# Kernel tuning notes

Hardware: AMD Instinct MI355X
Metric: run time of the kernel (lower is better)

## Reference

```python
import jax, jax.numpy as jnp
import numpy as np

EPS = 1e-7  # K.epsilon()
ROUTINGS = 3


def squash(v, axis=-1):
    s2 = jnp.sum(jnp.square(v), axis=axis, keepdims=True)
    scale = s2 / (1.0 + s2) / jnp.sqrt(s2 + EPS)
    return scale * v


def setup_inputs() -> dict:
    key = jax.random.key(0)
    k1, k2 = jax.random.split(key)
    B, Ni, Di, No, Do = 64, 2048, 16, 32, 16
    inputs = jax.random.normal(k1, (B, Ni, Di), dtype=jnp.float32)
    # glorot-uniform-ish scale for W
    limit = np.sqrt(6.0 / (Di + Do)).astype(np.float32)
    W = jax.random.uniform(k2, (1, Ni, No, Do, Di), dtype=jnp.float32,
                           minval=-limit, maxval=limit)
    return {"inputs": inputs, "W": W}


def reference(inputs, W):
    # inputs: [B, Ni, Di]; W: [1, Ni, No, Do, Di]
    # inputs_hat[b,n,o,d] = sum_i W[n,o,d,i] * inputs[b,n,i]  -> [B, Ni, No, Do]
    inputs_hat = jnp.einsum('bni,nodi->bnod', inputs, W[0])
    B, Ni, No, _ = inputs_hat.shape
    b = jnp.zeros((B, Ni, No), dtype=inputs_hat.dtype)
    outputs = None
    for i in range(ROUTINGS):
        c = jax.nn.softmax(b, axis=2)              # [B, Ni, No]
        s = jnp.einsum('bnod,bno->bod', inputs_hat, c)  # weighted sum over Ni
        outputs = squash(s)                        # [B, No, Do]
        if i < ROUTINGS - 1:
            # NOTE: faithful to source — update uses sum over Do of c-weighted
            # inputs_hat (does NOT use `outputs`).
            b = b + jnp.sum(inputs_hat * c[..., None], axis=-1)
    return outputs
```

## Files before the change

kernel.cpp:

```cpp
#include <hip/hip_runtime.h>
#include <cmath>


#define NI 2048
#define NGROUPS 256
#define NPER 8

typedef short bf16x8 __attribute__((ext_vector_type(8)));
typedef float f32x4 __attribute__((ext_vector_type(4)));

static __device__ __forceinline__ unsigned cvt_pk_bf16(float a, float b) {
  unsigned r;
  asm("v_cvt_pk_bf16_f32 %0, %1, %2" : "=v"(r) : "v"(a), "v"(b));
  return r;
}
static __device__ __forceinline__ void split4_pk(float4 v, uint2& hi, uint2& lo) {
  hi.x = cvt_pk_bf16(v.x, v.y);
  hi.y = cvt_pk_bf16(v.z, v.w);
  float r0 = v.x - __uint_as_float(hi.x << 16);
  float r1 = v.y - __uint_as_float(hi.x & 0xFFFF0000u);
  float r2 = v.z - __uint_as_float(hi.y << 16);
  float r3 = v.w - __uint_as_float(hi.y & 0xFFFF0000u);
  lo.x = cvt_pk_bf16(r0, r1);
  lo.y = cvt_pk_bf16(r2, r3);
}
static __device__ __forceinline__ int swz8(int r, int u) {
  return r * 8 + ((u ^ ((r >> 2) & 1)) << 2);
}

#define WAOFF 0
#define XBOFF 8192
#define HOFF  8704
#define C2OFF 9760
#define LDSZ  10816
__global__ __launch_bounds__(512, 4) void caps_fused_kernel(
    const float* __restrict__ x, const float* __restrict__ W,
    float* __restrict__ partial)
{
  const int bx = blockIdx.x;
  const int xcd = bx & 7, slot = bx >> 3;
  const int ng = xcd * 32 + (slot >> 1);
  const int bh = slot & 1;
  const int t = threadIdx.x;
  const int wv = t >> 6, l = t & 63;
  const int q = l >> 4, dq = l & 15, qh = q & 1, s_a = q >> 1;
  const int bt = wv & 1, oq = wv >> 1;

  __shared__ __align__(16) float lds[LDSZ];
  float* WA  = lds + WAOFF;
  float* XB  = lds + XBOFF;
  float* hS  = lds + HOFF;
  float* c2S = lds + C2OFF;

  float sacc[8][4];
  #pragma unroll
  for (int oo = 0; oo < 8; ++oo)
    { sacc[oo][0] = 0.f; sacc[oo][1] = 0.f; sacc[oo][2] = 0.f; sacc[oo][3] = 0.f; }

  const int n0 = ng * NPER;
  const int wd = (t >> 2) & 15, wi4 = t & 3;
  const int wu = wi4 >> 1, wsub = (wi4 & 1) * 2;
  const int xb = t >> 2, xi4 = t & 3;
  const int xu = xi4 >> 1, xsub = (xi4 & 1) * 2;

  float4 wreg[4];
  float4 xreg = make_float4(0.f, 0.f, 0.f, 0.f);
  #pragma unroll
  for (int c = 0; c < 4; ++c)
    wreg[c] = *(const float4*)(W + (size_t)n0 * 8192 + c * 2048 + 4 * t);
  if (t < 128)
    xreg = *(const float4*)(x + (size_t)(bh * 32 + xb) * (NI * 16) + n0 * 16 + xi4 * 4);

  #pragma unroll
  for (int c = 0; c < 4; ++c) {
    uint2 hi, lo;
    split4_pk(wreg[c], hi, lo);
    const int rh = (c * 8 + wv) * 32 + wd;
    *(uint2*)&WA[swz8(rh, wu) + wsub] = hi;
    *(uint2*)&WA[swz8(rh + 16, wu) + wsub] = lo;
  }
  if (t < 128) {
    uint2 hi, lo;
    split4_pk(xreg, hi, lo);
    *(uint2*)&XB[swz8(xb, xu) + xsub] = hi;
    *(uint2*)&XB[swz8(32 + xb, xu) + xsub] = lo;
  }
  __syncthreads();

  {
    const size_t nb = (size_t)(n0 + 1);
    #pragma unroll
    for (int c = 0; c < 4; ++c)
      wreg[c] = *(const float4*)(W + nb * 8192 + c * 2048 + 4 * t);
    if (t < 128)
      xreg = *(const float4*)(x + (size_t)(bh * 32 + xb) * (NI * 16) + nb * 16 + xi4 * 4);
  }

  #pragma unroll 1
  for (int nn = 0; nn < NPER; ++nn) {
    f32x4 Dv[8];
    {
      bf16x8 B0 = *(const bf16x8*)&XB[swz8(bt * 16 + dq, qh)];
      bf16x8 B1 = *(const bf16x8*)&XB[swz8(32 + bt * 16 + dq, qh)];
      #pragma unroll
      for (int oo = 0; oo < 8; ++oo) {
        const int o = oq * 8 + oo;
        bf16x8 A = *(const bf16x8*)&WA[swz8(o * 32 + s_a * 16 + dq, qh)];
        f32x4 D = {0.f, 0.f, 0.f, 0.f};
        D = __builtin_amdgcn_mfma_f32_16x16x32_bf16(A, B0, D, 0, 0, 0);
        D = __builtin_amdgcn_mfma_f32_16x16x32_bf16(A, B1, D, 0, 0, 0);
        Dv[oo] = D;
        float hs = D[0] + D[1] + D[2] + D[3];
        hs += __shfl_xor(hs, 16);
        hs += __shfl_xor(hs, 32);
        if (q == 0) hS[(bt * 16 + dq) * 33 + o] = hs;
      }
    }
    __syncthreads();

    if (nn < NPER - 1) {
      #pragma unroll
      for (int c = 0; c < 4; ++c) {
        uint2 hi, lo;
        split4_pk(wreg[c], hi, lo);
        const int rh = (c * 8 + wv) * 32 + wd;
        *(uint2*)&WA[swz8(rh, wu) + wsub] = hi;
        *(uint2*)&WA[swz8(rh + 16, wu) + wsub] = lo;
      }
      if (t < 128) {
        uint2 hi, lo;
        split4_pk(xreg, hi, lo);
        *(uint2*)&XB[swz8(xb, xu) + xsub] = hi;
        *(uint2*)&XB[swz8(32 + xb, xu) + xsub] = lo;
      }
    }

    {
      const int bl = t >> 4, op = t & 15;
      const float h0 = hS[bl * 33 + op];
      const float h1 = hS[bl * 33 + op + 16];
      const float b10 = h0 * 0.03125f, b11 = h1 * 0.03125f;
      float mx = fmaxf(b10, b11);
      mx = fmaxf(mx, __shfl_xor(mx, 1)); mx = fmaxf(mx, __shfl_xor(mx, 2));
      mx = fmaxf(mx, __shfl_xor(mx, 4)); mx = fmaxf(mx, __shfl_xor(mx, 8));
      const float e0 = __expf(b10 - mx), e1 = __expf(b11 - mx);
      float S = e0 + e1;
      S += __shfl_xor(S, 1); S += __shfl_xor(S, 2);
      S += __shfl_xor(S, 4); S += __shfl_xor(S, 8);
      const float inv = 1.0f / S;
      const float b20 = b10 + e0 * inv * h0, b21 = b11 + e1 * inv * h1;
      float mx2 = fmaxf(b20, b21);
      mx2 = fmaxf(mx2, __shfl_xor(mx2, 1)); mx2 = fmaxf(mx2, __shfl_xor(mx2, 2));
      mx2 = fmaxf(mx2, __shfl_xor(mx2, 4)); mx2 = fmaxf(mx2, __shfl_xor(mx2, 8));
      const float e20 = __expf(b20 - mx2), e21 = __expf(b21 - mx2);
      float S2 = e20 + e21;
      S2 += __shfl_xor(S2, 1); S2 += __shfl_xor(S2, 2);
      S2 += __shfl_xor(S2, 4); S2 += __shfl_xor(S2, 8);
      const float inv2 = 1.0f / S2;
      c2S[op * 33 + bl] = e20 * inv2;
      c2S[(op + 16) * 33 + bl] = e21 * inv2;
    }

    if (nn < NPER - 2) {
      const size_t nb = (size_t)(n0 + nn + 2);
      #pragma unroll
      for (int c = 0; c < 4; ++c)
        wreg[c] = *(const float4*)(W + nb * 8192 + c * 2048 + 4 * t);
      if (t < 128)
        xreg = *(const float4*)(x + (size_t)(bh * 32 + xb) * (NI * 16) + nb * 16 + xi4 * 4);
    }
    __syncthreads();

    #pragma unroll
    for (int oo = 0; oo < 8; ++oo) {
      const int o = oq * 8 + oo;
      const float c = c2S[o * 33 + bt * 16 + dq];
      sacc[oo][0] += c * Dv[oo][0]; sacc[oo][1] += c * Dv[oo][1];
      sacc[oo][2] += c * Dv[oo][2]; sacc[oo][3] += c * Dv[oo][3];
    }
  }

  float* pb = partial + (size_t)ng * 32768
            + (size_t)(bh * 32 + bt * 16 + dq) * 512 + q * 4;
  #pragma unroll
  for (int oo = 0; oo < 8; ++oo) {
    const int o = oq * 8 + oo;
    *(float4*)(pb + o * 16)
        = make_float4(sacc[oo][0], sacc[oo][1], sacc[oo][2], sacc[oo][3]);
  }
}

__global__ __launch_bounds__(256) void caps_reduce_kernel(
    const float* __restrict__ partial, float* __restrict__ out)
{
  const int t = threadIdx.x;
  const int w4 = t >> 6, ln = t & 63;
  const int pair = blockIdx.x * 4 + w4;
  const int b = pair >> 5, o = pair & 31;
  const int d = ln & 15, cg = ln >> 4;
  const float* p = partial + (size_t)b * 512 + o * 16 + d;
  float s = 0.f;
  #pragma unroll 8
  for (int gg = cg; gg < NGROUPS; gg += 4) s += p[(size_t)gg * 32768];
  s += __shfl_xor(s, 16); s += __shfl_xor(s, 32);
  float s2 = s * s;
  s2 += __shfl_xor(s2, 1); s2 += __shfl_xor(s2, 2);
  s2 += __shfl_xor(s2, 4); s2 += __shfl_xor(s2, 8);
  float scale = s2 / (1.0f + s2) / sqrtf(s2 + 1e-7f);
  if (ln < 16) out[(size_t)b * 512 + o * 16 + d] = scale * s;
}

extern "C" void kernel_launch(void* const* d_in, const int* in_sizes, int n_in,
                              void* d_out, int out_size, void* d_ws, size_t ws_size,
                              hipStream_t stream) {
  const float* x = (const float*)d_in[0];
  const float* W = (const float*)d_in[1];
  if (in_sizes[0] != 64 * 2048 * 16) { const float* tmp = x; x = W; W = tmp; }
  float* out = (float*)d_out;

  float* partial = (float*)d_ws;

  caps_fused_kernel<<<512, 512, 0, stream>>>(x, W, partial);
  caps_reduce_kernel<<<512, 256, 0, stream>>>(partial, out);
}
```

Baseline: 125.0 us.

## Preload all x slices into LDS upfront, raise MFMA priority, widen reduce kernel

The fused kernel now loads and bf16-splits the x tiles for all eight capsules of a group into LDS once at the start, instead of streaming one per iteration through registers with only 128 threads. The MFMA section is wrapped in s_setprio to favour matrix issue. The reduce kernel gives each (b,o) pair its own 256-thread block and sums through an LDS tree, so it issues more parallel loads across a 4x larger grid. The larger LDS footprint may lower occupancy, and the startup load adds latency before the first compute.

```diff
diff --git a/kernel.cpp b/kernel.cpp
--- a/kernel.cpp
+++ b/kernel.cpp
@@ -29,10 +29,10 @@
 }
 
 #define WAOFF 0
-#define XBOFF 8192
-#define HOFF  8704
-#define C2OFF 9760
-#define LDSZ  10816
+#define XLOFF 8192
+#define HOFF  12288
+#define C2OFF 13344
+#define LDSZ  14400
 __global__ __launch_bounds__(512, 4) void caps_fused_kernel(
     const float* __restrict__ x, const float* __restrict__ W,
     float* __restrict__ partial)
@@ -48,7 +48,7 @@
 
   __shared__ __align__(16) float lds[LDSZ];
   float* WA  = lds + WAOFF;
-  float* XB  = lds + XBOFF;
+  float* XL  = lds + XLOFF;
   float* hS  = lds + HOFF;
   float* c2S = lds + C2OFF;
 
@@ -60,16 +60,25 @@
   const int n0 = ng * NPER;
   const int wd = (t >> 2) & 15, wi4 = t & 3;
   const int wu = wi4 >> 1, wsub = (wi4 & 1) * 2;
-  const int xb = t >> 2, xi4 = t & 3;
-  const int xu = xi4 >> 1, xsub = (xi4 & 1) * 2;
 
   float4 wreg[4];
-  float4 xreg = make_float4(0.f, 0.f, 0.f, 0.f);
   #pragma unroll
   for (int c = 0; c < 4; ++c)
     wreg[c] = *(const float4*)(W + (size_t)n0 * 8192 + c * 2048 + 4 * t);
-  if (t < 128)
-    xreg = *(const float4*)(x + (size_t)(bh * 32 + xb) * (NI * 16) + n0 * 16 + xi4 * 4);
+
+  #pragma unroll
+  for (int m = 0; m < 2; ++m) {
+    const int idx = m * 512 + t;
+    const int pb = idx >> 5, pn = (idx >> 2) & 7, pi4 = idx & 3;
+    float4 v = *(const float4*)(x + (size_t)(bh * 32 + pb) * (NI * 16)
+                                 + (n0 + pn) * 16 + pi4 * 4);
+    uint2 hi, lo;
+    split4_pk(v, hi, lo);
+    const int pu = pi4 >> 1, psub = (pi4 & 1) * 2;
+    float* XLn = XL + pn * 512;
+    *(uint2*)&XLn[swz8(pb, pu) + psub] = hi;
+    *(uint2*)&XLn[swz8(32 + pb, pu) + psub] = lo;
+  }
 
   #pragma unroll
   for (int c = 0; c < 4; ++c) {
@@ -79,12 +88,6 @@
     *(uint2*)&WA[swz8(rh, wu) + wsub] = hi;
     *(uint2*)&WA[swz8(rh + 16, wu) + wsub] = lo;
   }
-  if (t < 128) {
-    uint2 hi, lo;
-    split4_pk(xreg, hi, lo);
-    *(uint2*)&XB[swz8(xb, xu) + xsub] = hi;
-    *(uint2*)&XB[swz8(32 + xb, xu) + xsub] = lo;
-  }
   __syncthreads();
 
   {
@@ -92,16 +95,16 @@
     #pragma unroll
     for (int c = 0; c < 4; ++c)
       wreg[c] = *(const float4*)(W + nb * 8192 + c * 2048 + 4 * t);
-    if (t < 128)
-      xreg = *(const float4*)(x + (size_t)(bh * 32 + xb) * (NI * 16) + nb * 16 + xi4 * 4);
   }
 
   #pragma unroll 1
   for (int nn = 0; nn < NPER; ++nn) {
     f32x4 Dv[8];
     {
-      bf16x8 B0 = *(const bf16x8*)&XB[swz8(bt * 16 + dq, qh)];
-      bf16x8 B1 = *(const bf16x8*)&XB[swz8(32 + bt * 16 + dq, qh)];
+      const float* XLn = XL + nn * 512;
+      __builtin_amdgcn_s_setprio(1);
+      bf16x8 B0 = *(const bf16x8*)&XLn[swz8(bt * 16 + dq, qh)];
+      bf16x8 B1 = *(const bf16x8*)&XLn[swz8(32 + bt * 16 + dq, qh)];
       #pragma unroll
       for (int oo = 0; oo < 8; ++oo) {
         const int o = oq * 8 + oo;
@@ -115,6 +118,7 @@
         hs += __shfl_xor(hs, 32);
         if (q == 0) hS[(bt * 16 + dq) * 33 + o] = hs;
       }
+      __builtin_amdgcn_s_setprio(0);
     }
     __syncthreads();
 
@@ -126,12 +130,6 @@
         const int rh = (c * 8 + wv) * 32 + wd;
         *(uint2*)&WA[swz8(rh, wu) + wsub] = hi;
         *(uint2*)&WA[swz8(rh + 16, wu) + wsub] = lo;
-      }
-      if (t < 128) {
-        uint2 hi, lo;
-        split4_pk(xreg, hi, lo);
-        *(uint2*)&XB[swz8(xb, xu) + xsub] = hi;
-        *(uint2*)&XB[swz8(32 + xb, xu) + xsub] = lo;
       }
     }
 
@@ -166,8 +164,6 @@
       #pragma unroll
       for (int c = 0; c < 4; ++c)
         wreg[c] = *(const float4*)(W + nb * 8192 + c * 2048 + 4 * t);
-      if (t < 128)
-        xreg = *(const float4*)(x + (size_t)(bh * 32 + xb) * (NI * 16) + nb * 16 + xi4 * 4);
     }
     __syncthreads();
 
@@ -194,20 +190,27 @@
     const float* __restrict__ partial, float* __restrict__ out)
 {
   const int t = threadIdx.x;
-  const int w4 = t >> 6, ln = t & 63;
-  const int pair = blockIdx.x * 4 + w4;
+  const int pair = blockIdx.x;
   const int b = pair >> 5, o = pair & 31;
-  const int d = ln & 15, cg = ln >> 4;
+  const int d = t & 15, g16 = t >> 4;
   const float* p = partial + (size_t)b * 512 + o * 16 + d;
   float s = 0.f;
-  #pragma unroll 8
-  for (int gg = cg; gg < NGROUPS; gg += 4) s += p[(size_t)gg * 32768];
-  s += __shfl_xor(s, 16); s += __shfl_xor(s, 32);
-  float s2 = s * s;
-  s2 += __shfl_xor(s2, 1); s2 += __shfl_xor(s2, 2);
-  s2 += __shfl_xor(s2, 4); s2 += __shfl_xor(s2, 8);
-  float scale = s2 / (1.0f + s2) / sqrtf(s2 + 1e-7f);
-  if (ln < 16) out[(size_t)b * 512 + o * 16 + d] = scale * s;
+  #pragma unroll
+  for (int k = 0; k < 16; ++k)
+    s += p[(size_t)(g16 + k * 16) * 32768];
+  __shared__ float red[16][17];
+  red[g16][d] = s;
+  __syncthreads();
+  if (t < 16) {
+    float sd = 0.f;
+    #pragma unroll
+    for (int g = 0; g < 16; ++g) sd += red[g][t];
+    float s2 = sd * sd;
+    s2 += __shfl_xor(s2, 1); s2 += __shfl_xor(s2, 2);
+    s2 += __shfl_xor(s2, 4); s2 += __shfl_xor(s2, 8);
+    float scale = s2 / (1.0f + s2) / sqrtf(s2 + 1e-7f);
+    out[(size_t)b * 512 + o * 16 + t] = scale * sd;
+  }
 }
 
 extern "C" void kernel_launch(void* const* d_in, const int* in_sizes, int n_in,
@@ -221,5 +224,5 @@
   float* partial = (float*)d_ws;
 
   caps_fused_kernel<<<512, 512, 0, stream>>>(x, W, partial);
-  caps_reduce_kernel<<<512, 256, 0, stream>>>(partial, out);
-}
+  caps_reduce_kernel<<<2048, 256, 0, stream>>>(partial, out);
+}
```

New measurement: 126.6 us. No clear change (+1.3%).

## Double-buffer W tiles in LDS and load x directly into MFMA B registers

Applied to the files above, without the earlier changes.

W tiles now alternate between two LDS buffers. The next tile is written before the current tile's MFMAs run, which moves the bf16 split/store off the critical path between barriers. The x operand no longer goes through LDS: each lane loads its own 8 floats from global memory, splits them into bf16 hi/lo in registers and feeds them to the MFMA directly. The cost is more LDS per block (about 74KB versus 43KB), which may limit blocks per CU, and every lane now issues its own x loads, which repeats some x traffic across waves.

```diff
diff --git a/kernel.cpp b/kernel.cpp
--- a/kernel.cpp
+++ b/kernel.cpp
@@ -28,11 +28,11 @@
   return r * 8 + ((u ^ ((r >> 2) & 1)) << 2);
 }
 
-#define WAOFF 0
-#define XBOFF 8192
-#define HOFF  8704
-#define C2OFF 9760
-#define LDSZ  10816
+#define WA0OFF 0
+#define WA1OFF 8192
+#define HOFF  16384
+#define C2OFF 17440
+#define LDSZ  18496
 __global__ __launch_bounds__(512, 4) void caps_fused_kernel(
     const float* __restrict__ x, const float* __restrict__ W,
     float* __restrict__ partial)
@@ -47,8 +47,6 @@
   const int bt = wv & 1, oq = wv >> 1;
 
   __shared__ __align__(16) float lds[LDSZ];
-  float* WA  = lds + WAOFF;
-  float* XB  = lds + XBOFF;
   float* hS  = lds + HOFF;
   float* c2S = lds + C2OFF;
 
@@ -60,63 +58,34 @@
   const int n0 = ng * NPER;
   const int wd = (t >> 2) & 15, wi4 = t & 3;
   const int wu = wi4 >> 1, wsub = (wi4 & 1) * 2;
-  const int xb = t >> 2, xi4 = t & 3;
-  const int xu = xi4 >> 1, xsub = (xi4 & 1) * 2;
+  const float* xptr = x + (size_t)(bh * 32 + bt * 16 + dq) * (NI * 16) + qh * 8;
 
   float4 wreg[4];
-  float4 xreg = make_float4(0.f, 0.f, 0.f, 0.f);
   #pragma unroll
   for (int c = 0; c < 4; ++c)
     wreg[c] = *(const float4*)(W + (size_t)n0 * 8192 + c * 2048 + 4 * t);
-  if (t < 128)
-    xreg = *(const float4*)(x + (size_t)(bh * 32 + xb) * (NI * 16) + n0 * 16 + xi4 * 4);
-
-  #pragma unroll
-  for (int c = 0; c < 4; ++c) {
-    uint2 hi, lo;
-    split4_pk(wreg[c], hi, lo);
-    const int rh = (c * 8 + wv) * 32 + wd;
-    *(uint2*)&WA[swz8(rh, wu) + wsub] = hi;
-    *(uint2*)&WA[swz8(rh + 16, wu) + wsub] = lo;
+  float4 xa = *(const float4*)(xptr + n0 * 16);
+  float4 xb = *(const float4*)(xptr + n0 * 16 + 4);
+  {
+    float* WAn = lds + WA0OFF;
+    #pragma unroll
+    for (int c = 0; c < 4; ++c) {
+      uint2 hi, lo;
+      split4_pk(wreg[c], hi, lo);
+      const int rh = (c * 8 + wv) * 32 + wd;
+      *(uint2*)&WAn[swz8(rh, wu) + wsub] = hi;
+      *(uint2*)&WAn[swz8(rh + 16, wu) + wsub] = lo;
+    }
   }
-  if (t < 128) {
-    uint2 hi, lo;
-    split4_pk(xreg, hi, lo);
-    *(uint2*)&XB[swz8(xb, xu) + xsub] = hi;
-    *(uint2*)&XB[swz8(32 + xb, xu) + xsub] = lo;
-  }
+  #pragma unroll
+  for (int c = 0; c < 4; ++c)
+    wreg[c] = *(const float4*)(W + (size_t)(n0 + 1) * 8192 + c * 2048 + 4 * t);
   __syncthreads();
-
-  {
-    const size_t nb = (size_t)(n0 + 1);
-    #pragma unroll
-    for (int c = 0; c < 4; ++c)
-      wreg[c] = *(const float4*)(W + nb * 8192 + c * 2048 + 4 * t);
-    if (t < 128)
-      xreg = *(const float4*)(x + (size_t)(bh * 32 + xb) * (NI * 16) + nb * 16 + xi4 * 4);
-  }
 
   #pragma unroll 1
   for (int nn = 0; nn < NPER; ++nn) {
-    f32x4 Dv[8];
-    {
-      bf16x8 B0 = *(const bf16x8*)&XB[swz8(bt * 16 + dq, qh)];
-      bf16x8 B1 = *(const bf16x8*)&XB[swz8(32 + bt * 16 + dq, qh)];
-      #pragma unroll
-      for (int oo = 0; oo < 8; ++oo) {
-        const int o = oq * 8 + oo;
-        bf16x8 A = *(const bf16x8*)&WA[swz8(o * 32 + s_a * 16 + dq, qh)];
-        f32x4 D = {0.f, 0.f, 0.f, 0.f};
-        D = __builtin_amdgcn_mfma_f32_16x16x32_bf16(A, B0, D, 0, 0, 0);
-        D = __builtin_amdgcn_mfma_f32_16x16x32_bf16(A, B1, D, 0, 0, 0);
-        Dv[oo] = D;
-        float hs = D[0] + D[1] + D[2] + D[3];
-        hs += __shfl_xor(hs, 16);
-        hs += __shfl_xor(hs, 32);
-        if (q == 0) hS[(bt * 16 + dq) * 33 + o] = hs;
-      }
-    }
-    __syncthreads();
+    float* WAc = lds + ((nn & 1) ? WA1OFF : WA0OFF);
+    float* WAn = lds + ((nn & 1) ? WA0OFF : WA1OFF);
 
     if (nn < NPER - 1) {
       #pragma unroll
@@ -124,16 +93,57 @@
         uint2 hi, lo;
         split4_pk(wreg[c], hi, lo);
         const int rh = (c * 8 + wv) * 32 + wd;
-        *(uint2*)&WA[swz8(rh, wu) + wsub] = hi;
-        *(uint2*)&WA[swz8(rh + 16, wu) + wsub] = lo;
+        *(uint2*)&WAn[swz8(rh, wu) + wsub] = hi;
+        *(uint2*)&WAn[swz8(rh + 16, wu) + wsub] = lo;
       }
-      if (t < 128) {
-        uint2 hi, lo;
-        split4_pk(xreg, hi, lo);
-        *(uint2*)&XB[swz8(xb, xu) + xsub] = hi;
-        *(uint2*)&XB[swz8(32 + xb, xu) + xsub] = lo;
-      }
-    }
+    }
+    if (nn < NPER - 2) {
+      const size_t nb = (size_t)(n0 + nn + 2);
+      #pragma unroll
+      for (int c = 0; c < 4; ++c)
+        wreg[c] = *(const float4*)(W + nb * 8192 + c * 2048 + 4 * t);
+    }
+
+    bf16x8 B0, B1;
+    {
+      unsigned p0 = cvt_pk_bf16(xa.x, xa.y), p1 = cvt_pk_bf16(xa.z, xa.w);
+      unsigned p2 = cvt_pk_bf16(xb.x, xb.y), p3 = cvt_pk_bf16(xb.z, xb.w);
+      float r0 = xa.x - __uint_as_float(p0 << 16);
+      float r1 = xa.y - __uint_as_float(p0 & 0xFFFF0000u);
+      float r2 = xa.z - __uint_as_float(p1 << 16);
+      float r3 = xa.w - __uint_as_float(p1 & 0xFFFF0000u);
+      float r4 = xb.x - __uint_as_float(p2 << 16);
+      float r5 = xb.y - __uint_as_float(p2 & 0xFFFF0000u);
+      float r6 = xb.z - __uint_as_float(p3 << 16);
+      float r7 = xb.w - __uint_as_float(p3 & 0xFFFF0000u);
+      unsigned g0 = cvt_pk_bf16(r0, r1), g1 = cvt_pk_bf16(r2, r3);
+      unsigned g2 = cvt_pk_bf16(r4, r5), g3 = cvt_pk_bf16(r6, r7);
+      union U { unsigned u[4]; bf16x8 v; };
+      U u0; u0.u[0] = p0; u0.u[1] = p1; u0.u[2] = p2; u0.u[3] = p3;
+      U u1; u1.u[0] = g0; u1.u[1] = g1; u1.u[2] = g2; u1.u[3] = g3;
+      B0 = u0.v;
+      B1 = u1.v;
+    }
+    if (nn < NPER - 1) {
+      xa = *(const float4*)(xptr + (n0 + nn + 1) * 16);
+      xb = *(const float4*)(xptr + (n0 + nn + 1) * 16 + 4);
+    }
+
+    f32x4 Dv[8];
+    #pragma unroll
+    for (int oo = 0; oo < 8; ++oo) {
+      const int o = oq * 8 + oo;
+      bf16x8 A = *(const bf16x8*)&WAc[swz8(o * 32 + s_a * 16 + dq, qh)];
+      f32x4 D = {0.f, 0.f, 0.f, 0.f};
+      D = __builtin_amdgcn_mfma_f32_16x16x32_bf16(A, B0, D, 0, 0, 0);
+      D = __builtin_amdgcn_mfma_f32_16x16x32_bf16(A, B1, D, 0, 0, 0);
+      Dv[oo] = D;
+      float hs = D[0] + D[1] + D[2] + D[3];
+      hs += __shfl_xor(hs, 16);
+      hs += __shfl_xor(hs, 32);
+      if (q == 0) hS[(bt * 16 + dq) * 33 + o] = hs;
+    }
+    __syncthreads();
 
     {
       const int bl = t >> 4, op = t & 15;
@@ -160,15 +170,6 @@
       c2S[op * 33 + bl] = e20 * inv2;
       c2S[(op + 16) * 33 + bl] = e21 * inv2;
     }
-
-    if (nn < NPER - 2) {
-      const size_t nb = (size_t)(n0 + nn + 2);
-      #pragma unroll
-      for (int c = 0; c < 4; ++c)
-        wreg[c] = *(const float4*)(W + nb * 8192 + c * 2048 + 4 * t);
-      if (t < 128)
-        xreg = *(const float4*)(x + (size_t)(bh * 32 + xb) * (NI * 16) + nb * 16 + xi4 * 4);
-    }
     __syncthreads();
 
     #pragma unroll
```

New measurement: 132.1 us. 5.7% more time.
